# Kernel tuning notes

Measured on AMD Instinct MI355X. Metric: run time of the kernel, lower is better.

## Reference

```python
import jax, jax.numpy as jnp
import numpy as np

D_MODEL = 256
NHEAD = 8
D_HEAD = D_MODEL // NHEAD
DIM_FF = 1024
B, L = 4, 16384
LN_EPS = 1e-5


def _layernorm(x, g, b):
    mu = jnp.mean(x, axis=-1, keepdims=True)
    var = jnp.mean((x - mu) ** 2, axis=-1, keepdims=True)
    return (x - mu) * jax.lax.rsqrt(var + LN_EPS) * g + b


def _phi(x):
    # elu(x) + 1
    return jnp.where(x > 0, x + 1.0, jnp.exp(x))


def setup_inputs() -> dict:
    key = jax.random.key(0)
    ks = jax.random.split(key, 16)
    s_in = 1.0 / np.sqrt(D_MODEL)
    s_ff = 1.0 / np.sqrt(DIM_FF)
    inp = {
        "x": jax.random.normal(ks[0], (B, L, D_MODEL), dtype=jnp.float32),
        "Wq": jax.random.normal(ks[1], (D_MODEL, D_MODEL), dtype=jnp.float32) * s_in,
        "bq": jnp.zeros((D_MODEL,), jnp.float32),
        "Wk": jax.random.normal(ks[2], (D_MODEL, D_MODEL), dtype=jnp.float32) * s_in,
        "bk": jnp.zeros((D_MODEL,), jnp.float32),
        "Wv": jax.random.normal(ks[3], (D_MODEL, D_MODEL), dtype=jnp.float32) * s_in,
        "bv": jnp.zeros((D_MODEL,), jnp.float32),
        "Wo": jax.random.normal(ks[4], (D_MODEL, D_MODEL), dtype=jnp.float32) * s_in,
        "bo": jnp.zeros((D_MODEL,), jnp.float32),
        "W1": jax.random.normal(ks[5], (D_MODEL, DIM_FF), dtype=jnp.float32) * s_in,
        "b1": jnp.zeros((DIM_FF,), jnp.float32),
        "W2": jax.random.normal(ks[6], (DIM_FF, D_MODEL), dtype=jnp.float32) * s_ff,
        "b2": jnp.zeros((D_MODEL,), jnp.float32),
        "ln1_g": jnp.ones((D_MODEL,), jnp.float32),
        "ln1_b": jnp.zeros((D_MODEL,), jnp.float32),
        "ln2_g": jnp.ones((D_MODEL,), jnp.float32),
        "ln2_b": jnp.zeros((D_MODEL,), jnp.float32),
    }
    return inp


def reference(x, Wq, bq, Wk, bk, Wv, bv, Wo, bo, W1, b1, W2, b2, ln1_g, ln1_b, ln2_g, ln2_b):
    Bq, Lq, _ = x.shape
    q = (x @ Wq + bq).reshape(Bq, Lq, NHEAD, D_HEAD)
    k = (x @ Wk + bk).reshape(Bq, Lq, NHEAD, D_HEAD)
    v = (x @ Wv + bv).reshape(Bq, Lq, NHEAD, D_HEAD)
    q_phi = _phi(q)
    k_phi = _phi(k)
    # kv: [B, H, d, e]
    kv = jnp.einsum("blhd,blhe->bhde", k_phi, v)
    k_sum = k_phi.sum(axis=1)  # [B, H, d]
    z = 1.0 / (jnp.einsum("blhd,bhd->blh", q_phi, k_sum) + 1e-6)
    out = jnp.einsum("blhd,bhde,blh->blhe", q_phi, kv, z)
    out = out.reshape(Bq, Lq, D_MODEL) @ Wo + bo
    x = _layernorm(x + out, ln1_g, ln1_b)
    ff = jax.nn.relu(x @ W1 + b1) @ W2 + b2
    x = _layernorm(x + ff, ln2_g, ln2_b)
    return x
```

## Files before the change

kernel.cpp:

```cpp
#include <hip/hip_runtime.h>
#include <hip/hip_bf16.h>
#include <math.h>

#define NTOK   65536
#define L_SEQ  16384

typedef __bf16 bf16_t;
typedef bf16_t bf16x8 __attribute__((ext_vector_type(8)));
typedef bf16_t bf16x4 __attribute__((ext_vector_type(4)));
typedef float  f32x4  __attribute__((ext_vector_type(4)));

__device__ inline float phi_f(float x) { return x > 0.f ? x + 1.f : __expf(x); }

__device__ inline float quad_sum(float v) {
    v += __shfl_xor(v, 1);
    v += __shfl_xor(v, 2);
    v += __shfl_xor(v, 4);
    v += __shfl_xor(v, 8);
    return v;
}

__device__ inline float ld_any(const void* p, size_t i, int f32) {
    return f32 ? ((const float*)p)[i] : (float)((const bf16_t*)p)[i];
}

__device__ inline void async_copy16(const bf16_t* g, bf16_t* l) {
    __builtin_amdgcn_global_load_lds(
        (const __attribute__((address_space(1))) unsigned int*)g,
        (__attribute__((address_space(3))) unsigned int*)l, 16, 0, 0);
}

__device__ inline void stage_swz(const bf16_t* __restrict__ g, bf16_t* lds,
                                 int tid, int nslot, int ulog2, int rowstride) {
    const int umask = (1 << ulog2) - 1;
    for (int s = tid; s < nslot; s += 256) {
        int n = s >> ulog2, j = s & umask;
        int u = j ^ (n & umask);
        async_copy16(g + (size_t)n * rowstride + u * 8, lds + (size_t)s * 8);
    }
}

__device__ inline bf16x8 rd_swz(const bf16_t* lds, int n, int u, int ulog2) {
    int j = u ^ (n & ((1 << ulog2) - 1));
    return *(const bf16x8*)&lds[(((size_t)n << ulog2) + j) * 8];
}

__device__ inline void stage_w2ff(const bf16_t* __restrict__ W2_t, int ch,
                                  bf16_t* lds, int tid) {
    for (int S = tid; S < 1024; S += 256) {
        int r = S >> 3, phys = S & 7;
        int u = phys ^ (r & 7);
        int n = ((u >> 2) << 7) + r;
        int ks = u & 3;
        async_copy16(W2_t + (size_t)n * 1024 + ch * 32 + ks * 8, lds + (size_t)S * 8);
    }
}

__device__ inline bf16x8 rd_w2ff(const bf16_t* lds, int n, int quad) {
    int r = n & 127;
    int u = ((n >> 7) << 2) + quad;
    int phys = u ^ (r & 7);
    return *(const bf16x8*)&lds[(size_t)(r * 8 + phys) * 8];
}

__device__ inline void hs_put(bf16_t* hs, int r, int c, bf16_t v) {
    int phys = (c >> 3) ^ (r & 15);
    hs[r * 128 + phys * 8 + (c & 7)] = v;
}
__device__ inline bf16x8 hs_get8(const bf16_t* hs, int r, int u) {
    int phys = u ^ (r & 15);
    return *(const bf16x8*)&hs[r * 128 + phys * 8];
}

__device__ inline void ld_afrags(const bf16_t* __restrict__ tile, int row, int q8,
                                 bf16x8 a[8]) {
#pragma unroll
    for (int kk = 0; kk < 8; ++kk)
        a[kk] = *(const bf16x8*)&tile[(size_t)row * 256 + kk * 32 + q8];
}

__global__ __launch_bounds__(256) void k_detect(const void* __restrict__ xraw,
                                                int* __restrict__ flag) {
    __shared__ int bad;
    if (threadIdx.x == 0) bad = 0;
    __syncthreads();
    const bf16_t* xb = (const bf16_t*)xraw;
    int mybad = 0;
#pragma unroll
    for (int j = 0; j < 16; ++j) {
        float v = fabsf((float)xb[threadIdx.x + 256 * j]);
        if (!(v <= 1000.f)) mybad = 1;
    }
    if (mybad) atomicOr(&bad, 1);
    __syncthreads();
    if (threadIdx.x == 0) *flag = bad;
}

__global__ __launch_bounds__(256) void k_convert(const void* __restrict__ xraw,
                                                 const int* __restrict__ flag,
                                                 bf16_t* __restrict__ xbf) {
    const int f = *flag;
    size_t i = ((size_t)blockIdx.x * 256 + threadIdx.x) * 4;
    if (f) {
        f32x4 v = *(const f32x4*)((const float*)xraw + i);
        bf16x4 o;
#pragma unroll
        for (int j = 0; j < 4; ++j) o[j] = (bf16_t)v[j];
        *(bf16x4*)&xbf[i] = o;
    } else {
        *(bf16x4*)&xbf[i] = *(const bf16x4*)((const bf16_t*)xraw + i);
    }
}

__global__ __launch_bounds__(256) void k_prep(
    const void* __restrict__ Wq, const void* __restrict__ Wk,
    const void* __restrict__ Wv, const void* __restrict__ Wo,
    const void* __restrict__ W1, const void* __restrict__ W2,
    const void* __restrict__ bq, const void* __restrict__ bk,
    const void* __restrict__ bv, const void* __restrict__ bo,
    const void* __restrict__ b1, const void* __restrict__ b2,
    const void* __restrict__ g1, const void* __restrict__ be1,
    const void* __restrict__ g2, const void* __restrict__ be2,
    const int* __restrict__ flag,
    bf16_t* __restrict__ Wqkv_t, bf16_t* __restrict__ Wo_t,
    bf16_t* __restrict__ W1_t, bf16_t* __restrict__ W2_t,
    bf16_t* __restrict__ pbuf, float* __restrict__ kvbuf) {
    const int f = *flag;
    int idx = blockIdx.x * 256 + threadIdx.x;
    if (idx < 196608) {
        int n = idx >> 8, k = idx & 255;
        float v;
        if (n < 256)      v = ld_any(Wq, k * 256 + n, f);
        else if (n < 512) v = ld_any(Wk, k * 256 + (n - 256), f);
        else              v = ld_any(Wv, k * 256 + (n - 512), f);
        Wqkv_t[idx] = (bf16_t)v;
    } else if (idx < 262144) {
        int i = idx - 196608; int n = i >> 8, k = i & 255;
        Wo_t[i] = (bf16_t)ld_any(Wo, k * 256 + n, f);
    } else if (idx < 524288) {
        int i = idx - 262144; int n = i >> 8, k = i & 255;
        W1_t[i] = (bf16_t)ld_any(W1, k * 1024 + n, f);
    } else if (idx < 786432) {
        int i = idx - 524288; int n = i >> 10, k = i & 1023;
        W2_t[i] = (bf16_t)ld_any(W2, k * 256 + n, f);
    } else if (idx < 820224) {
        kvbuf[idx - 786432] = 0.f;
    } else if (idx < 823552) {
        int i = idx - 820224;
        float v;
        if (i < 256)        v = ld_any(bq, i, f);
        else if (i < 512)   v = ld_any(bk, i - 256, f);
        else if (i < 768)   v = ld_any(bv, i - 512, f);
        else if (i < 1024)  v = ld_any(bo, i - 768, f);
        else if (i < 2048)  v = ld_any(b1, i - 1024, f);
        else if (i < 2304)  v = ld_any(b2, i - 2048, f);
        else if (i < 2560)  v = ld_any(g1, i - 2304, f);
        else if (i < 2816)  v = ld_any(be1, i - 2560, f);
        else if (i < 3072)  v = ld_any(g2, i - 2816, f);
        else                v = ld_any(be2, i - 3072, f);
        pbuf[i] = (bf16_t)v;
    }
}

__global__ __launch_bounds__(256, 3) void k_qkv(
    const bf16_t* __restrict__ x, const bf16_t* __restrict__ Wqkv_t,
    const bf16_t* __restrict__ pbuf, bf16_t* __restrict__ q_phi) {
    const int mt = blockIdx.x, nt = blockIdx.y;
    const int tid = threadIdx.x, wave = tid >> 6, lane = tid & 63;
    const int l15 = lane & 15, quad = lane >> 4, q8 = quad * 8;
    __shared__ __align__(16) bf16_t bs[128 * 256];
    const int m0 = mt * 128;
    bf16x8 a[2][8];
    ld_afrags(x + (size_t)m0 * 256,        wave * 16 + l15, q8, a[0]);
    ld_afrags(x + (size_t)(m0 + 64) * 256, wave * 16 + l15, q8, a[1]);
    stage_swz(Wqkv_t + (size_t)nt * 128 * 256, bs, tid, 4096, 5, 256);
    __syncthreads();
    f32x4 acc[2][8] = {};
#pragma unroll
    for (int kk = 0; kk < 8; ++kk) {
#pragma unroll
        for (int s = 0; s < 8; ++s) {
            bf16x8 b = rd_swz(bs, s * 16 + l15, kk * 4 + quad, 5);
            acc[0][s] = __builtin_amdgcn_mfma_f32_16x16x32_bf16(a[0][kk], b, acc[0][s], 0, 0, 0);
            acc[1][s] = __builtin_amdgcn_mfma_f32_16x16x32_bf16(a[1][kk], b, acc[1][s], 0, 0, 0);
        }
    }
#pragma unroll
    for (int s = 0; s < 8; ++s) {
        int ng = nt * 128 + s * 16 + l15;
        float bias = (float)pbuf[ng];
#pragma unroll
        for (int mm = 0; mm < 2; ++mm) {
#pragma unroll
            for (int r = 0; r < 4; ++r) {
                int m = m0 + mm * 64 + wave * 16 + quad * 4 + r;
                q_phi[(size_t)m * 256 + ng] = (bf16_t)phi_f(acc[mm][s][r] + bias);
            }
        }
    }
}

__global__ __launch_bounds__(256, 4) void k_kv(
    const bf16_t* __restrict__ x, const bf16_t* __restrict__ Wqkv_t,
    const bf16_t* __restrict__ pbuf, float* __restrict__ kvpart) {
    const int mt = blockIdx.x, hg = blockIdx.y;
    const int tid = threadIdx.x, wave = tid >> 6, lane = tid & 63;
    const int l15 = lane & 15, quad = lane >> 4, q8 = quad * 8;
    __shared__ __align__(16) bf16_t stg[8192];
    __shared__ __align__(16) bf16_t hsK[4096];
    __shared__ __align__(16) bf16_t hsV[4096];
    __shared__ float ksred[4][32];
    const int m0 = mt * 128;
    const int b = m0 >> 14;
    bf16x8 a[2][8];
    ld_afrags(x + (size_t)m0 * 256,        wave * 16 + l15, q8, a[0]);
    ld_afrags(x + (size_t)(m0 + 64) * 256, wave * 16 + l15, q8, a[1]);
    const int td = wave >> 1, te = wave & 1;
    for (int h4 = 0; h4 < 4; ++h4) {
        const int head = hg * 4 + h4;
        float* dst = kvpart + ((size_t)(b * 8 + head) * 128 + (mt & 127)) * 1056;
        stage_swz(Wqkv_t + (size_t)(256 + head * 32) * 256, stg, tid, 1024, 5, 256);
        __syncthreads();
        {
            f32x4 acck[2][2] = {};
#pragma unroll
            for (int kk = 0; kk < 8; ++kk) {
#pragma unroll
                for (int s = 0; s < 2; ++s) {
                    bf16x8 bb = rd_swz(stg, s * 16 + l15, kk * 4 + quad, 5);
                    acck[0][s] = __builtin_amdgcn_mfma_f32_16x16x32_bf16(a[0][kk], bb, acck[0][s], 0, 0, 0);
                    acck[1][s] = __builtin_amdgcn_mfma_f32_16x16x32_bf16(a[1][kk], bb, acck[1][s], 0, 0, 0);
                }
            }
#pragma unroll
            for (int s = 0; s < 2; ++s) {
                float bias = (float)pbuf[256 + head * 32 + s * 16 + l15];
                float kst = 0.f;
#pragma unroll
                for (int mm = 0; mm < 2; ++mm) {
#pragma unroll
                    for (int r = 0; r < 4; ++r) {
                        float v = phi_f(acck[mm][s][r] + bias);
                        kst += v;
                        int c = mm * 64 + wave * 16 + quad * 4 + r;
                        hs_put(hsK, s * 16 + l15, c, (bf16_t)v);
                    }
                }
                kst += __shfl_xor(kst, 16);
                kst += __shfl_xor(kst, 32);
                if (quad == 0) ksred[wave][s * 16 + l15] = kst;
            }
        }
        __syncthreads();
        stage_swz(Wqkv_t + (size_t)(512 + head * 32) * 256, stg, tid, 1024, 5, 256);
        __syncthreads();
        {
            f32x4 accv[2][2] = {};
#pragma unroll
            for (int kk = 0; kk < 8; ++kk) {
#pragma unroll
                for (int s = 0; s < 2; ++s) {
                    bf16x8 bb = rd_swz(stg, s * 16 + l15, kk * 4 + quad, 5);
                    accv[0][s] = __builtin_amdgcn_mfma_f32_16x16x32_bf16(a[0][kk], bb, accv[0][s], 0, 0, 0);
                    accv[1][s] = __builtin_amdgcn_mfma_f32_16x16x32_bf16(a[1][kk], bb, accv[1][s], 0, 0, 0);
                }
            }
#pragma unroll
            for (int s = 0; s < 2; ++s) {
                float bias = (float)pbuf[512 + head * 32 + s * 16 + l15];
#pragma unroll
                for (int mm = 0; mm < 2; ++mm) {
#pragma unroll
                    for (int r = 0; r < 4; ++r) {
                        int c = mm * 64 + wave * 16 + quad * 4 + r;
                        hs_put(hsV, s * 16 + l15, c, (bf16_t)(accv[mm][s][r] + bias));
                    }
                }
            }
        }
        __syncthreads();
        {
            f32x4 kvacc = {};
#pragma unroll
            for (int kk = 0; kk < 4; ++kk) {
                bf16x8 ak = hs_get8(hsK, td * 16 + l15, kk * 4 + quad);
                bf16x8 bv = hs_get8(hsV, te * 16 + l15, kk * 4 + quad);
                kvacc = __builtin_amdgcn_mfma_f32_16x16x32_bf16(ak, bv, kvacc, 0, 0, 0);
            }
            int e = te * 16 + l15;
            *(f32x4*)&dst[e * 32 + td * 16 + quad * 4] = kvacc;
        }
        if (tid < 32)
            dst[1024 + tid] = ksred[0][tid] + ksred[1][tid] + ksred[2][tid] + ksred[3][tid];
    }
}

__global__ __launch_bounds__(256) void k_kvred(const float* __restrict__ kvpart,
                                               float* __restrict__ kvbuf,
                                               bf16_t* __restrict__ kvbf) {
    const int bh = blockIdx.x;
    const int idx = blockIdx.y * 256 + threadIdx.x;
    if (idx >= 1056) return;
    const float* p = kvpart + (size_t)bh * 128 * 1056 + idx;
    float s = 0.f;
#pragma unroll 4
    for (int sl = 0; sl < 128; ++sl) s += p[(size_t)sl * 1056];
    kvbuf[(size_t)bh * 1056 + idx] = s;
    if (idx < 1024) kvbf[(size_t)bh * 1024 + idx] = (bf16_t)s;
}

__global__ __launch_bounds__(256, 2) void k_attn_wo_ln1(
    const bf16_t* __restrict__ q_phi, const bf16_t* __restrict__ kvbf,
    const float* __restrict__ kvbuf, const bf16_t* __restrict__ Wo_t,
    const bf16_t* __restrict__ pbuf, const void* __restrict__ xraw,
    const int* __restrict__ flag, bf16_t* __restrict__ x1) {
    const int f = *flag;
    const int mt = blockIdx.x;
    const int tid = threadIdx.x, wave = tid >> 6, lane = tid & 63;
    const int l15 = lane & 15, quad = lane >> 4, q8 = quad * 8;
    __shared__ __align__(16) bf16_t sm0[8192];
    __shared__ __align__(16) bf16_t sm1[16896];
    const int m0 = mt * 128;
    const int b = m0 >> 14;
    stage_swz(Wo_t, sm0, tid, 1024, 5, 256);
    bf16_t* hs = sm1 + wave * (16 * 264);
    const bf16_t* kvb = kvbf + (size_t)b * 8192;
    const float*  ksb = kvbuf + (size_t)b * 8448;
    bf16x8 a2[2][8];
#pragma unroll
    for (int mm = 0; mm < 2; ++mm) {
        bf16x8 a[8];
        ld_afrags(q_phi + (size_t)(m0 + mm * 64) * 256, wave * 16 + l15, q8, a);
#pragma unroll
        for (int h = 0; h < 8; ++h) {
            f32x4 ks0 = *(const f32x4*)&ksb[h * 1056 + 1024 + q8];
            f32x4 ks1 = *(const f32x4*)&ksb[h * 1056 + 1024 + q8 + 4];
            float den = 0.f;
#pragma unroll
            for (int j = 0; j < 4; ++j) den += (float)a[h][j] * ks0[j];
#pragma unroll
            for (int j = 0; j < 4; ++j) den += (float)a[h][4 + j] * ks1[j];
            den += __shfl_xor(den, 16);
            den += __shfl_xor(den, 32);
            float z = 1.f / (den + 1e-6f);
            float zr[4];
#pragma unroll
            for (int r = 0; r < 4; ++r) zr[r] = __shfl(z, quad * 4 + r, 16);
            bf16x8 b0 = *(const bf16x8*)&kvb[h * 1024 + l15 * 32 + q8];
            bf16x8 b1 = *(const bf16x8*)&kvb[h * 1024 + (16 + l15) * 32 + q8];
            f32x4 at0 = {}, at1 = {};
            at0 = __builtin_amdgcn_mfma_f32_16x16x32_bf16(a[h], b0, at0, 0, 0, 0);
            at1 = __builtin_amdgcn_mfma_f32_16x16x32_bf16(a[h], b1, at1, 0, 0, 0);
#pragma unroll
            for (int r = 0; r < 4; ++r) {
                hs[(quad * 4 + r) * 264 + h * 32 + l15]      = (bf16_t)(at0[r] * zr[r]);
                hs[(quad * 4 + r) * 264 + h * 32 + 16 + l15] = (bf16_t)(at1[r] * zr[r]);
            }
        }
#pragma unroll
        for (int kk = 0; kk < 8; ++kk)
            a2[mm][kk] = *(const bf16x8*)&hs[l15 * 264 + kk * 32 + q8];
    }
    __syncthreads();
    f32x4 acc[2][16] = {};
    for (int nc = 0; nc < 8; ++nc) {
        if (nc < 7) stage_swz(Wo_t + (size_t)(nc + 1) * 32 * 256,
                              (nc & 1) ? sm0 : sm1, tid, 1024, 5, 256);
        const bf16_t* buf = (nc & 1) ? sm1 : sm0;
#pragma unroll
        for (int kk = 0; kk < 8; ++kk) {
#pragma unroll
            for (int s = 0; s < 2; ++s) {
                bf16x8 bb = rd_swz(buf, s * 16 + l15, kk * 4 + quad, 5);
                acc[0][nc * 2 + s] = __builtin_amdgcn_mfma_f32_16x16x32_bf16(a2[0][kk], bb, acc[0][nc * 2 + s], 0, 0, 0);
                acc[1][nc * 2 + s] = __builtin_amdgcn_mfma_f32_16x16x32_bf16(a2[1][kk], bb, acc[1][nc * 2 + s], 0, 0, 0);
            }
        }
        __syncthreads();
    }
#pragma unroll
    for (int mm = 0; mm < 2; ++mm) {
        float s1[4] = {}, s2[4] = {};
#pragma unroll
        for (int s = 0; s < 16; ++s) {
            int n = s * 16 + l15;
            float bias = (float)pbuf[768 + n];
#pragma unroll
            for (int r = 0; r < 4; ++r) {
                int m = m0 + mm * 64 + wave * 16 + quad * 4 + r;
                float val = acc[mm][s][r] + bias + ld_any(xraw, (size_t)m * 256 + n, f);
                acc[mm][s][r] = val;
                s1[r] += val; s2[r] += val * val;
            }
        }
#pragma unroll
        for (int r = 0; r < 4; ++r) {
            float ts = quad_sum(s1[r]), ts2 = quad_sum(s2[r]);
            float mu = ts * (1.f / 256.f);
            float rs = rsqrtf(ts2 * (1.f / 256.f) - mu * mu + 1e-5f);
            s1[r] = mu; s2[r] = rs;
        }
#pragma unroll
        for (int s = 0; s < 16; ++s) {
            int n = s * 16 + l15;
            float gn = (float)pbuf[2304 + n], bn = (float)pbuf[2560 + n];
#pragma unroll
            for (int r = 0; r < 4; ++r) {
                int m = m0 + mm * 64 + wave * 16 + quad * 4 + r;
                x1[(size_t)m * 256 + n] = (bf16_t)((acc[mm][s][r] - s1[r]) * s2[r] * gn + bn);
            }
        }
    }
}

__global__ __launch_bounds__(256, 2) void k_ff_ln2(
    const bf16_t* __restrict__ x1, const bf16_t* __restrict__ W1_t,
    const bf16_t* __restrict__ W2_t, const bf16_t* __restrict__ pbuf,
    const int* __restrict__ flag, void* __restrict__ out) {
    const int f32o = *flag;
    const int mt = blockIdx.x;
    const int tid = threadIdx.x, wave = tid >> 6, lane = tid & 63;
    const int l15 = lane & 15, quad = lane >> 4, q8 = quad * 8;
    __shared__ __align__(16) bf16_t w1s[2][8192];
    __shared__ __align__(16) bf16_t w2s[2][8192];
    __shared__ __align__(16) bf16_t hs[4][2][16][40];
    const int m0 = mt * 128 + wave * 32;
    bf16x8 a[2][8];
    ld_afrags(x1 + (size_t)m0 * 256, l15,      q8, a[0]);
    ld_afrags(x1 + (size_t)m0 * 256, 16 + l15, q8, a[1]);
    stage_swz(W1_t, w1s[0], tid, 1024, 5, 256);
    stage_w2ff(W2_t, 0, w2s[0], tid);
    __syncthreads();
    f32x4 acc[2][16] = {};
    for (int ch = 0; ch < 32; ++ch) {
        const int cur = ch & 1;
        if (ch < 31) {
            stage_swz(W1_t + (size_t)(ch + 1) * 32 * 256, w1s[cur ^ 1], tid, 1024, 5, 256);
            stage_w2ff(W2_t, ch + 1, w2s[cur ^ 1], tid);
        }
        f32x4 h0[2] = {}, h1[2] = {};
#pragma unroll
        for (int kk = 0; kk < 8; ++kk) {
#pragma unroll
            for (int s = 0; s < 2; ++s) {
                bf16x8 b = rd_swz(w1s[cur], s * 16 + l15, kk * 4 + quad, 5);
                h0[s] = __builtin_amdgcn_mfma_f32_16x16x32_bf16(a[0][kk], b, h0[s], 0, 0, 0);
                h1[s] = __builtin_amdgcn_mfma_f32_16x16x32_bf16(a[1][kk], b, h1[s], 0, 0, 0);
            }
        }
#pragma unroll
        for (int s = 0; s < 2; ++s) {
            float bias = (float)pbuf[1024 + ch * 32 + s * 16 + l15];
#pragma unroll
            for (int r = 0; r < 4; ++r) {
                float v0 = h0[s][r] + bias;
                float v1 = h1[s][r] + bias;
                hs[wave][0][quad * 4 + r][s * 16 + l15] = (bf16_t)(v0 > 0.f ? v0 : 0.f);
                hs[wave][1][quad * 4 + r][s * 16 + l15] = (bf16_t)(v1 > 0.f ? v1 : 0.f);
            }
        }
        bf16x8 a2_0 = *(const bf16x8*)&hs[wave][0][l15][q8];
        bf16x8 a2_1 = *(const bf16x8*)&hs[wave][1][l15][q8];
#pragma unroll
        for (int s = 0; s < 16; ++s) {
            bf16x8 b0 = rd_w2ff(w2s[cur], s * 16 + l15, quad);
            acc[0][s] = __builtin_amdgcn_mfma_f32_16x16x32_bf16(a2_0, b0, acc[0][s], 0, 0, 0);
            acc[1][s] = __builtin_amdgcn_mfma_f32_16x16x32_bf16(a2_1, b0, acc[1][s], 0, 0, 0);
        }
        __syncthreads();
    }
#pragma unroll
    for (int mm = 0; mm < 2; ++mm) {
        float s1[4] = {}, s2[4] = {};
#pragma unroll
        for (int s = 0; s < 16; ++s) {
            int n = s * 16 + l15;
            float bias = (float)pbuf[2048 + n];
#pragma unroll
            for (int r = 0; r < 4; ++r) {
                int m = m0 + mm * 16 + quad * 4 + r;
                float val = acc[mm][s][r] + bias + (float)x1[(size_t)m * 256 + n];
                acc[mm][s][r] = val;
                s1[r] += val; s2[r] += val * val;
            }
        }
#pragma unroll
        for (int r = 0; r < 4; ++r) {
            float ts = quad_sum(s1[r]), ts2 = quad_sum(s2[r]);
            float mu = ts * (1.f / 256.f);
            float rs = rsqrtf(ts2 * (1.f / 256.f) - mu * mu + 1e-5f);
            s1[r] = mu; s2[r] = rs;
        }
#pragma unroll
        for (int s = 0; s < 16; ++s) {
            int n = s * 16 + l15;
            float gn = (float)pbuf[2816 + n], bn = (float)pbuf[3072 + n];
#pragma unroll
            for (int r = 0; r < 4; ++r) {
                int m = m0 + mm * 16 + quad * 4 + r;
                float val = (acc[mm][s][r] - s1[r]) * s2[r] * gn + bn;
                if (f32o) ((float*)out)[(size_t)m * 256 + n] = val;
                else      ((bf16_t*)out)[(size_t)m * 256 + n] = (bf16_t)val;
            }
        }
    }
}

extern "C" void kernel_launch(void* const* d_in, const int* in_sizes, int n_in,
                              void* d_out, int out_size, void* d_ws, size_t ws_size,
                              hipStream_t stream) {
    char* ws = (char*)d_ws;
    int*    flag   = (int*)ws;
    bf16_t* xbf    = (bf16_t*)(ws + 256);
    bf16_t* Wqkv_t = (bf16_t*)(ws + 33554688);
    bf16_t* Wo_t   = (bf16_t*)(ws + 33947904);
    bf16_t* W1_t   = (bf16_t*)(ws + 34078976);
    bf16_t* W2_t   = (bf16_t*)(ws + 34603264);
    bf16_t* pbuf   = (bf16_t*)(ws + 35127552);
    float*  kvbuf  = (float*)(ws + 35134208);
    bf16_t* bufQ   = (bf16_t*)(ws + 35269376);
    bf16_t* kvbf   = bufQ + (size_t)NTOK * 256;
    float*  kvpart = (float*)(ws + 35269376 + 2u * NTOK * 256 + 65536);
    bf16_t* bufX1  = bufQ;

    k_detect<<<1, 256, 0, stream>>>(d_in[0], flag);
    k_convert<<<16384, 256, 0, stream>>>(d_in[0], flag, xbf);
    k_prep<<<3217, 256, 0, stream>>>(d_in[1], d_in[3], d_in[5], d_in[7],
                                     d_in[9], d_in[11],
                                     d_in[2], d_in[4], d_in[6], d_in[8],
                                     d_in[10], d_in[12],
                                     d_in[13], d_in[14], d_in[15], d_in[16],
                                     flag, Wqkv_t, Wo_t, W1_t, W2_t, pbuf, kvbuf);
    k_qkv<<<dim3(512, 2), 256, 0, stream>>>(xbf, Wqkv_t, pbuf, bufQ);
    k_kv<<<dim3(512, 2), 256, 0, stream>>>(xbf, Wqkv_t, pbuf, kvpart);
    k_kvred<<<dim3(32, 5), 256, 0, stream>>>(kvpart, kvbuf, kvbf);
    k_attn_wo_ln1<<<512, 256, 0, stream>>>(bufQ, kvbf, kvbuf, Wo_t, pbuf,
                                           d_in[0], flag, bufX1);
    k_ff_ln2<<<512, 256, 0, stream>>>(bufX1, W1_t, W2_t, pbuf, flag, d_out);
}
```

Before: 364.6 us.

## Fuse Q projection into k_kv kernel and raise MFMA priority in FF loop

Removes the separate k_qkv launch and computes the phi(Q) projection inside k_kv, reusing the x A-fragments already loaded in registers and staging Q weight slices in 32-column chunks through the existing small shared buffer. This avoids reading x a second time and saves one kernel launch. The cost is extra __syncthreads and smaller staging chunks, which lengthen k_kv. It also wraps the MFMA loops in the FF kernel with s_setprio so matrix work gets scheduling priority over other waves.

```diff
diff --git a/kernel.cpp b/kernel.cpp
--- a/kernel.cpp
+++ b/kernel.cpp
@@ -162,47 +162,10 @@
     }
 }
 
-__global__ __launch_bounds__(256, 3) void k_qkv(
-    const bf16_t* __restrict__ x, const bf16_t* __restrict__ Wqkv_t,
-    const bf16_t* __restrict__ pbuf, bf16_t* __restrict__ q_phi) {
-    const int mt = blockIdx.x, nt = blockIdx.y;
-    const int tid = threadIdx.x, wave = tid >> 6, lane = tid & 63;
-    const int l15 = lane & 15, quad = lane >> 4, q8 = quad * 8;
-    __shared__ __align__(16) bf16_t bs[128 * 256];
-    const int m0 = mt * 128;
-    bf16x8 a[2][8];
-    ld_afrags(x + (size_t)m0 * 256,        wave * 16 + l15, q8, a[0]);
-    ld_afrags(x + (size_t)(m0 + 64) * 256, wave * 16 + l15, q8, a[1]);
-    stage_swz(Wqkv_t + (size_t)nt * 128 * 256, bs, tid, 4096, 5, 256);
-    __syncthreads();
-    f32x4 acc[2][8] = {};
-#pragma unroll
-    for (int kk = 0; kk < 8; ++kk) {
-#pragma unroll
-        for (int s = 0; s < 8; ++s) {
-            bf16x8 b = rd_swz(bs, s * 16 + l15, kk * 4 + quad, 5);
-            acc[0][s] = __builtin_amdgcn_mfma_f32_16x16x32_bf16(a[0][kk], b, acc[0][s], 0, 0, 0);
-            acc[1][s] = __builtin_amdgcn_mfma_f32_16x16x32_bf16(a[1][kk], b, acc[1][s], 0, 0, 0);
-        }
-    }
-#pragma unroll
-    for (int s = 0; s < 8; ++s) {
-        int ng = nt * 128 + s * 16 + l15;
-        float bias = (float)pbuf[ng];
-#pragma unroll
-        for (int mm = 0; mm < 2; ++mm) {
-#pragma unroll
-            for (int r = 0; r < 4; ++r) {
-                int m = m0 + mm * 64 + wave * 16 + quad * 4 + r;
-                q_phi[(size_t)m * 256 + ng] = (bf16_t)phi_f(acc[mm][s][r] + bias);
-            }
-        }
-    }
-}
-
 __global__ __launch_bounds__(256, 4) void k_kv(
     const bf16_t* __restrict__ x, const bf16_t* __restrict__ Wqkv_t,
-    const bf16_t* __restrict__ pbuf, float* __restrict__ kvpart) {
+    const bf16_t* __restrict__ pbuf, bf16_t* __restrict__ q_phi,
+    float* __restrict__ kvpart) {
     const int mt = blockIdx.x, hg = blockIdx.y;
     const int tid = threadIdx.x, wave = tid >> 6, lane = tid & 63;
     const int l15 = lane & 15, quad = lane >> 4, q8 = quad * 8;
@@ -215,6 +178,35 @@
     bf16x8 a[2][8];
     ld_afrags(x + (size_t)m0 * 256,        wave * 16 + l15, q8, a[0]);
     ld_afrags(x + (size_t)(m0 + 64) * 256, wave * 16 + l15, q8, a[1]);
+    for (int c = 0; c < 4; ++c) {
+        const int col0 = hg * 128 + c * 32;
+        stage_swz(Wqkv_t + (size_t)col0 * 256, stg, tid, 1024, 5, 256);
+        __syncthreads();
+        f32x4 accq[2][2] = {};
+#pragma unroll
+        for (int kk = 0; kk < 8; ++kk) {
+#pragma unroll
+            for (int s = 0; s < 2; ++s) {
+                bf16x8 bb = rd_swz(stg, s * 16 + l15, kk * 4 + quad, 5);
+                accq[0][s] = __builtin_amdgcn_mfma_f32_16x16x32_bf16(a[0][kk], bb, accq[0][s], 0, 0, 0);
+                accq[1][s] = __builtin_amdgcn_mfma_f32_16x16x32_bf16(a[1][kk], bb, accq[1][s], 0, 0, 0);
+            }
+        }
+#pragma unroll
+        for (int s = 0; s < 2; ++s) {
+            int col = col0 + s * 16 + l15;
+            float bias = (float)pbuf[col];
+#pragma unroll
+            for (int mm = 0; mm < 2; ++mm) {
+#pragma unroll
+                for (int r = 0; r < 4; ++r) {
+                    int m = m0 + mm * 64 + wave * 16 + quad * 4 + r;
+                    q_phi[(size_t)m * 256 + col] = (bf16_t)phi_f(accq[mm][s][r] + bias);
+                }
+            }
+        }
+        __syncthreads();
+    }
     const int td = wave >> 1, te = wave & 1;
     for (int h4 = 0; h4 < 4; ++h4) {
         const int head = hg * 4 + h4;
@@ -439,6 +431,7 @@
             stage_w2ff(W2_t, ch + 1, w2s[cur ^ 1], tid);
         }
         f32x4 h0[2] = {}, h1[2] = {};
+        __builtin_amdgcn_s_setprio(1);
 #pragma unroll
         for (int kk = 0; kk < 8; ++kk) {
 #pragma unroll
@@ -448,6 +441,7 @@
                 h1[s] = __builtin_amdgcn_mfma_f32_16x16x32_bf16(a[1][kk], b, h1[s], 0, 0, 0);
             }
         }
+        __builtin_amdgcn_s_setprio(0);
 #pragma unroll
         for (int s = 0; s < 2; ++s) {
             float bias = (float)pbuf[1024 + ch * 32 + s * 16 + l15];
@@ -461,12 +455,14 @@
         }
         bf16x8 a2_0 = *(const bf16x8*)&hs[wave][0][l15][q8];
         bf16x8 a2_1 = *(const bf16x8*)&hs[wave][1][l15][q8];
+        __builtin_amdgcn_s_setprio(1);
 #pragma unroll
         for (int s = 0; s < 16; ++s) {
             bf16x8 b0 = rd_w2ff(w2s[cur], s * 16 + l15, quad);
             acc[0][s] = __builtin_amdgcn_mfma_f32_16x16x32_bf16(a2_0, b0, acc[0][s], 0, 0, 0);
             acc[1][s] = __builtin_amdgcn_mfma_f32_16x16x32_bf16(a2_1, b0, acc[1][s], 0, 0, 0);
         }
+        __builtin_amdgcn_s_setprio(0);
         __syncthreads();
     }
 #pragma unroll
@@ -531,8 +527,7 @@
                                      d_in[10], d_in[12],
                                      d_in[13], d_in[14], d_in[15], d_in[16],
                                      flag, Wqkv_t, Wo_t, W1_t, W2_t, pbuf, kvbuf);
-    k_qkv<<<dim3(512, 2), 256, 0, stream>>>(xbf, Wqkv_t, pbuf, bufQ);
-    k_kv<<<dim3(512, 2), 256, 0, stream>>>(xbf, Wqkv_t, pbuf, kvpart);
+    k_kv<<<dim3(512, 2), 256, 0, stream>>>(xbf, Wqkv_t, pbuf, bufQ, kvpart);
     k_kvred<<<dim3(32, 5), 256, 0, stream>>>(kvpart, kvbuf, kvbf);
     k_attn_wo_ln1<<<512, 256, 0, stream>>>(bufQ, kvbf, kvbuf, Wo_t, pbuf,
                                            d_in[0], flag, bufX1);
```

After: 367.9 us. About the same (+0.9%).
